# Optimization experiments

Measured on AMD Instinct MI355X. Metric: run time of the kernel, lower is better.

The kernel has to match this reference:

```python
import jax, jax.numpy as jnp
import numpy as np

N_NODES = 100000
N_EDGES = 1600000
IN_FEATS = 128
HIDDEN = 128
N_CLASSES = 40
EPS = 1e-5  # BatchNorm1d default eps


def setup_inputs():
    key = jax.random.key(0)
    ks = jax.random.split(key, 12)
    s_in = 1.0 / np.sqrt(IN_FEATS)
    s_h = 1.0 / np.sqrt(HIDDEN)
    return {
        "feat": jax.random.normal(ks[0], (N_NODES, IN_FEATS), jnp.float32),
        "src": jax.random.randint(ks[1], (N_EDGES,), 0, N_NODES, jnp.int32),
        "dst": jax.random.randint(ks[2], (N_EDGES,), 0, N_NODES, jnp.int32),
        # GraphConv weights, stored (out, in) as in the torch module
        "w0": jax.random.normal(ks[3], (HIDDEN, IN_FEATS), jnp.float32) * s_in,
        "w1": jax.random.normal(ks[4], (HIDDEN, HIDDEN), jnp.float32) * s_h,
        "w2": jax.random.normal(ks[5], (N_CLASSES, HIDDEN), jnp.float32) * s_h,
        "b2": jnp.zeros((N_CLASSES,), jnp.float32),  # bias only on last layer
        # skip-connection linears (use_linear=True, bias=False)
        "l0": jax.random.normal(ks[6], (HIDDEN, IN_FEATS), jnp.float32) * s_in,
        "l1": jax.random.normal(ks[7], (HIDDEN, HIDDEN), jnp.float32) * s_h,
        "l2": jax.random.normal(ks[8], (N_CLASSES, HIDDEN), jnp.float32) * s_h,
        # BatchNorm affine params for the two hidden layers
        "g0": jnp.ones((HIDDEN,), jnp.float32),
        "beta0": jnp.zeros((HIDDEN,), jnp.float32),
        "g1": jnp.ones((HIDDEN,), jnp.float32),
        "beta1": jnp.zeros((HIDDEN,), jnp.float32),
    }


def _spmm(h, src, dst):
    # copy_u + sum aggregation: out[d] = sum_{e: dst[e]==d} h[src[e]]
    return jax.ops.segment_sum(h[src], dst, num_segments=N_NODES)


def gcn_forward(feat, src, dst, w0, w1, w2, b2, l0, l1, l2, g0, beta0, g1, beta1):
    ones = jnp.ones((src.shape[0],), jnp.float32)
    out_deg = jnp.clip(jax.ops.segment_sum(ones, src, num_segments=N_NODES), 1.0)
    in_deg = jnp.clip(jax.ops.segment_sum(ones, dst, num_segments=N_NODES), 1.0)
    out_norm = out_deg ** -0.5  # norm='both', applied to src features
    in_norm = in_deg ** -0.5    # norm='both', applied to aggregated result

    def conv(h, W, bias, in_gt_out):
        hs = h * out_norm[:, None]
        if in_gt_out:  # in_feats > out_feats: project first, then aggregate
            rst = _spmm(hs @ W.T, src, dst)
        else:          # aggregate first, then project
            rst = _spmm(hs, src, dst) @ W.T
        rst = rst * in_norm[:, None]
        if bias is not None:
            rst = rst + bias
        return rst

    def bn(x, g, b):
        mu = x.mean(0)
        var = x.var(0)  # biased variance, matches BN training-mode normalization
        return (x - mu) * jax.lax.rsqrt(var + EPS) * g + b

    h = feat  # dropout in eval mode = identity
    h = jax.nn.relu(bn(conv(h, w0, None, IN_FEATS > HIDDEN) + h @ l0.T, g0, beta0))
    h = jax.nn.relu(bn(conv(h, w1, None, False) + h @ l1.T, g1, beta1))
    h = conv(h, w2, b2, HIDDEN > N_CLASSES) + h @ l2.T
    return h


def reference(feat, src, dst, w0, w1, w2, b2, l0, l1, l2, g0, beta0, g1, beta1):
    return gcn_forward(feat, src, dst, w0, w1, w2, b2, l0, l1, l2, g0, beta0, g1, beta1)
```

## Files before the change

### kernel.cpp

```cpp
#include <hip/hip_runtime.h>
#include <hip/hip_fp16.h>
#include <cstdint>
#include <cstddef>

#define N_NODES 100000
#define N_EDGES 1600000
#define EPS 1e-5f

typedef _Float16 half8 __attribute__((ext_vector_type(8)));
typedef float floatx4 __attribute__((ext_vector_type(4)));

#define HCH 128
#define HRG 4
#define HBINS 32768
#define HWORDS (HBINS / 2)
#define HCHUNK (N_EDGES / HCH)
#define HCHUNK4 (HCHUNK / 4)

__global__ void k_hist_part(const int* __restrict__ keys, unsigned int* __restrict__ Hpart) {
  __shared__ unsigned int bins[HWORDS];
  int c = blockIdx.x % HCH, r = blockIdx.x / HCH;
  int base = r * HBINS;
  for (int i = threadIdx.x; i < HWORDS; i += 256) bins[i] = 0;
  __syncthreads();
  const int4* k4 = (const int4*)(keys + c * HCHUNK);
  for (int i = threadIdx.x; i < HCHUNK4; i += 256) {
    int4 k = k4[i];
    int a;
    a = k.x - base; if ((unsigned)a < (unsigned)HBINS) atomicAdd(&bins[a >> 1], 1u << ((a & 1) * 16));
    a = k.y - base; if ((unsigned)a < (unsigned)HBINS) atomicAdd(&bins[a >> 1], 1u << ((a & 1) * 16));
    a = k.z - base; if ((unsigned)a < (unsigned)HBINS) atomicAdd(&bins[a >> 1], 1u << ((a & 1) * 16));
    a = k.w - base; if ((unsigned)a < (unsigned)HBINS) atomicAdd(&bins[a >> 1], 1u << ((a & 1) * 16));
  }
  __syncthreads();
  unsigned int* outp = Hpart + ((size_t)blockIdx.x << 14);
  for (int i = threadIdx.x; i < HWORDS; i += 256) outp[i] = bins[i];
}

__global__ void k_hist_sum(const unsigned short* __restrict__ Hp, int* __restrict__ deg) {
  int b = blockIdx.x * 256 + threadIdx.x;
  if (b >= N_NODES) return;
  int r = b >> 15, lo = b & (HBINS - 1);
  const unsigned short* p = Hp + ((size_t)(r * HCH) << 15) + lo;
  unsigned int t = 0;
#pragma unroll 8
  for (int c = 0; c < HCH; ++c) t += p[(size_t)c << 15];
  deg[b] = (int)t;
}

__global__ void k_hist_scan(unsigned short* __restrict__ Hp, int* __restrict__ degd) {
  int b = blockIdx.x * 256 + threadIdx.x;
  if (b >= N_NODES) return;
  int r = b >> 15, lo = b & (HBINS - 1);
  unsigned short* p = Hp + ((size_t)(r * HCH) << 15) + lo;
  unsigned int t = 0;
#pragma unroll 8
  for (int c = 0; c < HCH; ++c) {
    unsigned int v = p[(size_t)c << 15];
    p[(size_t)c << 15] = (unsigned short)t;
    t += v;
  }
  degd[b] = (int)t;
}

__global__ void k_build(const int* __restrict__ src, const int* __restrict__ dst,
                        const unsigned short* __restrict__ Hbase,
                        const int* __restrict__ row_start, int* __restrict__ col) {
  __shared__ unsigned int cur[HWORDS];
  int c = blockIdx.x % HCH, r = blockIdx.x / HCH;
  int base = r * HBINS;
  for (int i = threadIdx.x; i < HWORDS; i += 256) cur[i] = 0;
  __syncthreads();
  const unsigned short* hb = Hbase + ((size_t)blockIdx.x << 15);
  const int4* d4 = (const int4*)(dst + c * HCHUNK);
  const int4* s4 = (const int4*)(src + c * HCHUNK);
  for (int i = threadIdx.x; i < HCHUNK4; i += 256) {
    int4 d = d4[i];
    int4 s = s4[i];
    int a;
    a = d.x - base;
    if ((unsigned)a < (unsigned)HBINS) {
      unsigned old = atomicAdd(&cur[a >> 1], 1u << ((a & 1) * 16));
      unsigned lr = (old >> ((a & 1) * 16)) & 0xffffu;
      col[row_start[d.x] + hb[a] + lr] = s.x;
    }
    a = d.y - base;
    if ((unsigned)a < (unsigned)HBINS) {
      unsigned old = atomicAdd(&cur[a >> 1], 1u << ((a & 1) * 16));
      unsigned lr = (old >> ((a & 1) * 16)) & 0xffffu;
      col[row_start[d.y] + hb[a] + lr] = s.y;
    }
    a = d.z - base;
    if ((unsigned)a < (unsigned)HBINS) {
      unsigned old = atomicAdd(&cur[a >> 1], 1u << ((a & 1) * 16));
      unsigned lr = (old >> ((a & 1) * 16)) & 0xffffu;
      col[row_start[d.z] + hb[a] + lr] = s.z;
    }
    a = d.w - base;
    if ((unsigned)a < (unsigned)HBINS) {
      unsigned old = atomicAdd(&cur[a >> 1], 1u << ((a & 1) * 16));
      unsigned lr = (old >> ((a & 1) * 16)) & 0xffffu;
      col[row_start[d.w] + hb[a] + lr] = s.w;
    }
  }
}

__global__ void k_norms(const int* __restrict__ degs, const int* __restrict__ degd,
                        float* out_norm, float* in_norm) {
  int i = blockIdx.x * 256 + threadIdx.x;
  if (i < N_NODES) {
    out_norm[i] = rsqrtf((float)max(degs[i], 1));
    in_norm[i]  = rsqrtf((float)max(degd[i], 1));
  }
}

__global__ void k_scan1(const int* __restrict__ degd, int* bsum) {
  __shared__ int s[256];
  int t = threadIdx.x;
  int i = blockIdx.x * 256 + t;
  s[t] = (i < N_NODES) ? degd[i] : 0;
  __syncthreads();
  for (int off = 128; off > 0; off >>= 1) {
    if (t < off) s[t] += s[t + off];
    __syncthreads();
  }
  if (t == 0) bsum[blockIdx.x] = s[0];
}

__global__ void k_scan2(int* bsum, int nb) {
  __shared__ int s[512];
  int t = threadIdx.x;
  int v = (t < nb) ? bsum[t] : 0;
  s[t] = v;
  __syncthreads();
  for (int off = 1; off < 512; off <<= 1) {
    int x = (t >= off) ? s[t - off] : 0;
    __syncthreads();
    s[t] += x;
    __syncthreads();
  }
  if (t < nb) bsum[t] = s[t] - v;
}

__global__ void k_scan3(const int* __restrict__ degd, const int* __restrict__ bsum,
                        int* row_start) {
  __shared__ int s[256];
  int t = threadIdx.x;
  int i = blockIdx.x * 256 + t;
  int v = (i < N_NODES) ? degd[i] : 0;
  s[t] = v;
  __syncthreads();
  for (int off = 1; off < 256; off <<= 1) {
    int x = (t >= off) ? s[t - off] : 0;
    __syncthreads();
    s[t] += x;
    __syncthreads();
  }
  if (i < N_NODES) row_start[i] = bsum[blockIdx.x] + s[t] - v;
  if (i == 0) row_start[N_NODES] = N_EDGES;
}

__global__ void k_feat2h(const float* __restrict__ feat, const float* __restrict__ out_norm,
                         unsigned short* __restrict__ H, unsigned short* __restrict__ F) {
  int i = blockIdx.x * 256 + threadIdx.x;
  if (i >= N_NODES * 32) return;
  float on = out_norm[i >> 5];
  float4 v = ((const float4*)feat)[i];
  ushort4 s, u;
  s.x = __half_as_ushort(__float2half_rn(v.x * on));
  s.y = __half_as_ushort(__float2half_rn(v.y * on));
  s.z = __half_as_ushort(__float2half_rn(v.z * on));
  s.w = __half_as_ushort(__float2half_rn(v.w * on));
  u.x = __half_as_ushort(__float2half_rn(v.x));
  u.y = __half_as_ushort(__float2half_rn(v.y));
  u.z = __half_as_ushort(__float2half_rn(v.z));
  u.w = __half_as_ushort(__float2half_rn(v.w));
  ((ushort4*)H)[i] = s;
  ((ushort4*)F)[i] = u;
}

__global__ void k_agg128h(const __half* __restrict__ H, const int* __restrict__ col,
                          const int* __restrict__ row_start,
                          const float* __restrict__ in_norm,
                          unsigned short* __restrict__ out16) {
  int wave = threadIdx.x >> 6;
  int lane = threadIdx.x & 63;
  int node = blockIdx.x * 4 + wave;
  if (node >= N_NODES) return;
  int q = lane >> 4;
  int sub = lane & 15;
  int s0 = row_start[node], s1 = row_start[node + 1];
  const uint4* hp = (const uint4*)H;
  float a[8];
#pragma unroll
  for (int j = 0; j < 8; ++j) a[j] = 0.f;
  int e = s0 + q;
  for (; e + 4 < s1; e += 8) {
    int c0 = col[e];
    int c1 = col[e + 4];
    uint4 u0 = hp[(size_t)c0 * 16 + sub];
    uint4 u1 = hp[(size_t)c1 * 16 + sub];
    const __half2* h0 = (const __half2*)&u0;
    const __half2* h1 = (const __half2*)&u1;
#pragma unroll
    for (int j = 0; j < 4; ++j) {
      float2 f0 = __half22float2(h0[j]);
      float2 f1 = __half22float2(h1[j]);
      a[2 * j] += f0.x + f1.x;
      a[2 * j + 1] += f0.y + f1.y;
    }
  }
  if (e < s1) {
    uint4 u = hp[(size_t)col[e] * 16 + sub];
    const __half2* h0 = (const __half2*)&u;
#pragma unroll
    for (int j = 0; j < 4; ++j) {
      float2 f = __half22float2(h0[j]);
      a[2 * j] += f.x;
      a[2 * j + 1] += f.y;
    }
  }
#pragma unroll
  for (int j = 0; j < 8; ++j) {
    a[j] += __shfl_xor(a[j], 16);
    a[j] += __shfl_xor(a[j], 32);
  }
  if (q == 0) {
    float sc = in_norm[node];
    __half2 o[4];
#pragma unroll
    for (int j = 0; j < 4; ++j)
      o[j] = __float22half2_rn(make_float2(a[2 * j] * sc, a[2 * j + 1] * sc));
    ((uint4*)out16)[(size_t)node * 16 + sub] = *(const uint4*)o;
  }
}

__launch_bounds__(256)
__global__ void k_gemm_dual16(const unsigned short* __restrict__ Xa,
                              const unsigned short* __restrict__ Xh,
                              const float* __restrict__ Wa, const float* __restrict__ Wh,
                              unsigned short* __restrict__ Out16, float* __restrict__ stats) {
  __shared__ __align__(16) unsigned short sX[64][136];
  __shared__ __align__(16) unsigned short sW[128][136];
  int t = threadIdx.x;
  int row0 = blockIdx.x * 64;
  int w = t >> 6, lane = t & 63;
  int q = lane >> 4, m = lane & 15;
  floatx4 acc[8];
#pragma unroll
  for (int i = 0; i < 8; ++i) acc[i] = (floatx4){0.f, 0.f, 0.f, 0.f};

  for (int phase = 0; phase < 2; ++phase) {
    const unsigned short* Xg = phase ? Xh : Xa;
    const float* Wg = phase ? Wh : Wa;
    __syncthreads();
    {
      int r = t >> 2;
      int c0 = (t & 3) * 4;
      const uint4* xr = (const uint4*)(Xg + (size_t)min(row0 + r, N_NODES - 1) * 128);
#pragma unroll
      for (int it = 0; it < 4; ++it) {
        uint4 v = xr[c0 + it];
        *(uint4*)&sX[r][(c0 + it) * 8] = v;
      }
    }
    {
      int n = t >> 1, h = (t & 1) * 64;
      const float4* wr = (const float4*)(Wg + (size_t)n * 128 + h);
#pragma unroll
      for (int it = 0; it < 16; ++it) {
        float4 v = wr[it];
        ushort4 o;
        o.x = __half_as_ushort(__float2half_rn(v.x));
        o.y = __half_as_ushort(__float2half_rn(v.y));
        o.z = __half_as_ushort(__float2half_rn(v.z));
        o.w = __half_as_ushort(__float2half_rn(v.w));
        *(ushort4*)&sW[n][h + it * 4] = o;
      }
    }
    __syncthreads();
#pragma unroll
    for (int ks = 0; ks < 4; ++ks) {
      int kk = ks * 32 + q * 8;
      half8 a = *(const half8*)&sX[w * 16 + m][kk];
#pragma unroll
      for (int t8 = 0; t8 < 8; ++t8) {
        half8 b = *(const half8*)&sW[t8 * 16 + m][kk];
        acc[t8] = __builtin_amdgcn_mfma_f32_16x16x32_f16(a, b, acc[t8], 0, 0, 0);
      }
    }
  }
  float ps[8], pq[8];
#pragma unroll
  for (int t8 = 0; t8 < 8; ++t8) {
    int colj = t8 * 16 + m;
    float s = 0.f, sq = 0.f;
#pragma unroll
    for (int i = 0; i < 4; ++i) {
      int row = row0 + w * 16 + q * 4 + i;
      if (row < N_NODES) {
        float v = acc[t8][i];
        s += v; sq += v * v;
        Out16[(size_t)row * 128 + colj] = __half_as_ushort(__float2half_rn(v));
      }
    }
    s += __shfl_xor(s, 16);
    s += __shfl_xor(s, 32);
    sq += __shfl_xor(sq, 16);
    sq += __shfl_xor(sq, 32);
    ps[t8] = s; pq[t8] = sq;
  }
  __syncthreads();
  float* pSum = (float*)&sX[0][0];
  float* pSq = pSum + 512;
  if (q == 0) {
#pragma unroll
    for (int t8 = 0; t8 < 8; ++t8) {
      pSum[w * 128 + t8 * 16 + m] = ps[t8];
      pSq[w * 128 + t8 * 16 + m] = pq[t8];
    }
  }
  __syncthreads();
  if (t < 128) {
    float s = (pSum[t] + pSum[128 + t]) + (pSum[256 + t] + pSum[384 + t]);
    float sq = (pSq[t] + pSq[128 + t]) + (pSq[256 + t] + pSq[384 + t]);
    atomicAdd(&stats[t], s);
    atomicAdd(&stats[128 + t], sq);
  }
}

__global__ void k_bnrelu16(const unsigned short* __restrict__ x16,
                           const float* __restrict__ stats,
                           const float* __restrict__ g, const float* __restrict__ b,
                           const float* __restrict__ out_norm,
                           unsigned short* __restrict__ H, unsigned short* __restrict__ F) {
  int i = blockIdx.x * 256 + threadIdx.x;
  if (i >= N_NODES * 16) return;
  int c8 = (i & 15) * 8;
  uint4 raw = ((const uint4*)x16)[i];
  const __half2* hp2 = (const __half2*)&raw;
  float v[8];
#pragma unroll
  for (int j = 0; j < 4; ++j) {
    float2 f = __half22float2(hp2[j]);
    v[2 * j] = f.x;
    v[2 * j + 1] = f.y;
  }
  const float inv = 1.f / (float)N_NODES;
#pragma unroll
  for (int j = 0; j < 8; ++j) {
    int c = c8 + j;
    float mu = stats[c] * inv;
    float var = stats[128 + c] * inv - mu * mu;
    float rs = rsqrtf(var + EPS);
    float y = (v[j] - mu) * rs * g[c] + b[c];
    v[j] = y > 0.f ? y : 0.f;
  }
  if (H) {
    float on = out_norm[i >> 4];
    ushort4 o[2];
#pragma unroll
    for (int j = 0; j < 8; ++j) ((unsigned short*)o)[j] = __half_as_ushort(__float2half_rn(v[j] * on));
    ((uint4*)H)[i] = *(const uint4*)o;
  }
  if (F) {
    ushort4 o[2];
#pragma unroll
    for (int j = 0; j < 8; ++j) ((unsigned short*)o)[j] = __half_as_ushort(__float2half_rn(v[j]));
    ((uint4*)F)[i] = *(const uint4*)o;
  }
}

__launch_bounds__(256)
__global__ void k_gemm2_16(const unsigned short* __restrict__ X,
                           const float* __restrict__ w2, const float* __restrict__ l2,
                           const float* __restrict__ b2,
                           const float* __restrict__ out_norm,
                           __half* __restrict__ p, float* __restrict__ out) {
  __shared__ __align__(16) unsigned short sX[64][136];
  __shared__ __align__(16) unsigned short sW[80][136];
  int t = threadIdx.x;
  int row0 = blockIdx.x * 64;
  int w = t >> 6, lane = t & 63;
  int q = lane >> 4, m = lane & 15;
  {
    int r = t >> 2;
    int c0 = (t & 3) * 4;
    const uint4* xr = (const uint4*)(X + (size_t)min(row0 + r, N_NODES - 1) * 128);
#pragma unroll
    for (int it = 0; it < 4; ++it) {
      uint4 v = xr[c0 + it];
      *(uint4*)&sX[r][(c0 + it) * 8] = v;
    }
  }
  {
#pragma unroll
    for (int it = 0; it < 10; ++it) {
      int i = it * 256 + t;
      int j = i >> 5;
      int kq = i & 31;
      const float* srcp = (j < 40) ? (w2 + (size_t)j * 128) : (l2 + (size_t)(j - 40) * 128);
      float4 v = ((const float4*)srcp)[kq];
      ushort4 o;
      o.x = __half_as_ushort(__float2half_rn(v.x));
      o.y = __half_as_ushort(__float2half_rn(v.y));
      o.z = __half_as_ushort(__float2half_rn(v.z));
      o.w = __half_as_ushort(__float2half_rn(v.w));
      *(ushort4*)&sW[j][kq * 4] = o;
    }
  }
  __syncthreads();
  floatx4 acc[5];
#pragma unroll
  for (int i = 0; i < 5; ++i) acc[i] = (floatx4){0.f, 0.f, 0.f, 0.f};
#pragma unroll
  for (int ks = 0; ks < 4; ++ks) {
    int kk = ks * 32 + q * 8;
    half8 a = *(const half8*)&sX[w * 16 + m][kk];
#pragma unroll
    for (int t5 = 0; t5 < 5; ++t5) {
      half8 b = *(const half8*)&sW[t5 * 16 + m][kk];
      acc[t5] = __builtin_amdgcn_mfma_f32_16x16x32_f16(a, b, acc[t5], 0, 0, 0);
    }
  }
#pragma unroll
  for (int t5 = 0; t5 < 5; ++t5) {
    int col = t5 * 16 + m;
#pragma unroll
    for (int i = 0; i < 4; ++i) {
      int row = row0 + w * 16 + q * 4 + i;
      if (row >= N_NODES) continue;
      if (col < 40) {
        p[(size_t)row * 40 + col] = __float2half_rn(out_norm[row] * acc[t5][i]);
      } else {
        out[(size_t)row * 40 + (col - 40)] = acc[t5][i] + b2[col - 40];
      }
    }
  }
}

__global__ void k_agg40h(const __half* __restrict__ p, const int* __restrict__ col,
                         const int* __restrict__ row_start,
                         const float* __restrict__ in_norm,
                         float* __restrict__ out) {
  int wave = threadIdx.x >> 6, lane = threadIdx.x & 63;
  int node = blockIdx.x * 4 + wave;
  if (node >= N_NODES) return;
  int s0 = row_start[node], s1 = row_start[node + 1];
  float a0 = 0.f, a1 = 0.f, a2 = 0.f, a3 = 0.f;
  int e = s0;
  for (; e + 4 <= s1; e += 4) {
    int sA = col[e], sB = col[e + 1], sC = col[e + 2], sD = col[e + 3];
    float vA = __half2float(p[(size_t)sA * 40 + lane]);
    float vB = __half2float(p[(size_t)sB * 40 + lane]);
    float vC = __half2float(p[(size_t)sC * 40 + lane]);
    float vD = __half2float(p[(size_t)sD * 40 + lane]);
    a0 += vA; a1 += vB; a2 += vC; a3 += vD;
  }
  for (; e < s1; ++e) {
    a0 += __half2float(p[(size_t)col[e] * 40 + lane]);
  }
  if (lane < 40) out[(size_t)node * 40 + lane] += in_norm[node] * ((a0 + a1) + (a2 + a3));
}

extern "C" void kernel_launch(void* const* d_in, const int* in_sizes, int n_in,
                              void* d_out, int out_size, void* d_ws, size_t ws_size,
                              hipStream_t stream) {
  const float* feat = (const float*)d_in[0];
  const int* src = (const int*)d_in[1];
  const int* dst = (const int*)d_in[2];
  const float* w0 = (const float*)d_in[3];
  const float* w1 = (const float*)d_in[4];
  const float* w2 = (const float*)d_in[5];
  const float* b2 = (const float*)d_in[6];
  const float* l0 = (const float*)d_in[7];
  const float* l1 = (const float*)d_in[8];
  const float* l2 = (const float*)d_in[9];
  const float* g0 = (const float*)d_in[10];
  const float* beta0 = (const float*)d_in[11];
  const float* g1 = (const float*)d_in[12];
  const float* beta1 = (const float*)d_in[13];
  float* out = (float*)d_out;

  char* ws = (char*)d_ws;
  size_t off = 0;
  auto alloc = [&](size_t bytes) {
    void* ptr = ws + off;
    off = (off + bytes + 255) & ~(size_t)255;
    return ptr;
  };
  unsigned short* A16 = (unsigned short*)alloc(2 * (size_t)N_NODES * 128);
  float* B = (float*)alloc(sizeof(float) * (size_t)N_NODES * 128);
  unsigned short* H = (unsigned short*)alloc(2 * (size_t)N_NODES * 128);
  unsigned short* F = (unsigned short*)alloc(2 * (size_t)N_NODES * 128);
  int* degs = (int*)alloc(sizeof(int) * N_NODES);
  int* degd = (int*)alloc(sizeof(int) * N_NODES);
  int* row_start = (int*)alloc(sizeof(int) * (N_NODES + 1));
  int* colb = (int*)alloc(sizeof(int) * N_EDGES);
  float* out_norm = (float*)alloc(sizeof(float) * N_NODES);
  float* in_norm = (float*)alloc(sizeof(float) * N_NODES);
  int* bsum = (int*)alloc(sizeof(int) * 512);
  float* stats = (float*)alloc(sizeof(float) * 256);

  unsigned int* Hpart = (unsigned int*)B;
  unsigned short* B16 = (unsigned short*)B;

  int nb = (N_NODES + 255) / 256;
  int hb = HCH * HRG;

  k_hist_part<<<hb, 256, 0, stream>>>(src, Hpart);
  k_hist_sum<<<nb, 256, 0, stream>>>((const unsigned short*)Hpart, degs);
  k_hist_part<<<hb, 256, 0, stream>>>(dst, Hpart);
  k_hist_scan<<<nb, 256, 0, stream>>>((unsigned short*)Hpart, degd);
  k_norms<<<nb, 256, 0, stream>>>(degs, degd, out_norm, in_norm);
  k_scan1<<<nb, 256, 0, stream>>>(degd, bsum);
  k_scan2<<<1, 512, 0, stream>>>(bsum, nb);
  k_scan3<<<nb, 256, 0, stream>>>(degd, bsum, row_start);
  k_build<<<hb, 256, 0, stream>>>(src, dst, (const unsigned short*)Hpart, row_start, colb);

  int ab = (N_NODES + 3) / 4;
  int gb = (N_NODES + 63) / 64;
  int fb = (N_NODES * 32 + 255) / 256;
  int hb16 = (N_NODES * 16 + 255) / 256;

  k_feat2h<<<fb, 256, 0, stream>>>(feat, out_norm, H, F);
  k_agg128h<<<ab, 256, 0, stream>>>((const __half*)H, colb, row_start, in_norm, A16);
  hipMemsetAsync(stats, 0, sizeof(float) * 256, stream);
  k_gemm_dual16<<<gb, 256, 0, stream>>>(A16, F, w0, l0, B16, stats);
  k_bnrelu16<<<hb16, 256, 0, stream>>>(B16, stats, g0, beta0, out_norm, H, F);

  k_agg128h<<<ab, 256, 0, stream>>>((const __half*)H, colb, row_start, in_norm, A16);
  hipMemsetAsync(stats, 0, sizeof(float) * 256, stream);
  k_gemm_dual16<<<gb, 256, 0, stream>>>(A16, F, w1, l1, B16, stats);
  k_bnrelu16<<<hb16, 256, 0, stream>>>(B16, stats, g1, beta1, out_norm,
                                       (unsigned short*)nullptr, F);

  __half* p = (__half*)A16;
  k_gemm2_16<<<gb, 256, 0, stream>>>(F, w2, l2, b2, out_norm, p, out);
  k_agg40h<<<ab, 256, 0, stream>>>(p, colb, row_start, in_norm, out);
}
```

Measured before the change: 572.2 us.

## Pre-convert weights to fp16, two-stage BN stats, pad final aggregation rows to 64

Weights are converted to fp16 once in a small kernel, so the GEMM blocks no longer convert fp32 weights per block. BN statistics are written as per-block partials and reduced by a separate kernel instead of global atomics. Tile loads are reorganised so a wave reads contiguous rows. The final-layer intermediate is padded to 64 halves per row and aggregated with 16-byte vector loads, eight edges in parallel per wave. This adds two extra launches and extra bytes for the padding.

```diff
diff --git a/kernel.cpp b/kernel.cpp
--- a/kernel.cpp
+++ b/kernel.cpp
@@ -158,6 +158,29 @@
   }
   if (i < N_NODES) row_start[i] = bsum[blockIdx.x] + s[t] - v;
   if (i == 0) row_start[N_NODES] = N_EDGES;
+}
+
+__global__ void k_w2h(const float* __restrict__ w0, const float* __restrict__ l0,
+                      const float* __restrict__ w1, const float* __restrict__ l1,
+                      const float* __restrict__ w2, const float* __restrict__ l2,
+                      unsigned short* __restrict__ W) {
+  int i = blockIdx.x * 256 + threadIdx.x;
+  if (i >= 18944) return;
+  int h = i * 4;
+  const float* src; int off;
+  if (h < 16384)      { src = w0; off = h; }
+  else if (h < 32768) { src = l0; off = h - 16384; }
+  else if (h < 49152) { src = w1; off = h - 32768; }
+  else if (h < 65536) { src = l1; off = h - 49152; }
+  else if (h < 70656) { src = w2; off = h - 65536; }
+  else                { src = l2; off = h - 70656; }
+  float4 v = *(const float4*)(src + off);
+  ushort4 o;
+  o.x = __half_as_ushort(__float2half_rn(v.x));
+  o.y = __half_as_ushort(__float2half_rn(v.y));
+  o.z = __half_as_ushort(__float2half_rn(v.z));
+  o.w = __half_as_ushort(__float2half_rn(v.w));
+  ((ushort4*)W)[i] = o;
 }
 
 __global__ void k_feat2h(const float* __restrict__ feat, const float* __restrict__ out_norm,
@@ -238,8 +261,8 @@
 __launch_bounds__(256)
 __global__ void k_gemm_dual16(const unsigned short* __restrict__ Xa,
                               const unsigned short* __restrict__ Xh,
-                              const float* __restrict__ Wa, const float* __restrict__ Wh,
-                              unsigned short* __restrict__ Out16, float* __restrict__ stats) {
+                              const unsigned short* __restrict__ W16,
+                              unsigned short* __restrict__ Out16, float* __restrict__ pstats) {
   __shared__ __align__(16) unsigned short sX[64][136];
   __shared__ __align__(16) unsigned short sW[128][136];
   int t = threadIdx.x;
@@ -252,30 +275,23 @@
 
   for (int phase = 0; phase < 2; ++phase) {
     const unsigned short* Xg = phase ? Xh : Xa;
-    const float* Wg = phase ? Wh : Wa;
     __syncthreads();
     {
-      int r = t >> 2;
-      int c0 = (t & 3) * 4;
-      const uint4* xr = (const uint4*)(Xg + (size_t)min(row0 + r, N_NODES - 1) * 128);
 #pragma unroll
       for (int it = 0; it < 4; ++it) {
-        uint4 v = xr[c0 + it];
-        *(uint4*)&sX[r][(c0 + it) * 8] = v;
+        int idx = it * 256 + t;
+        int r = idx >> 4, g = idx & 15;
+        const uint4* xr = (const uint4*)(Xg + (size_t)min(row0 + r, N_NODES - 1) * 128);
+        *(uint4*)&sX[r][g * 8] = xr[g];
       }
     }
     {
-      int n = t >> 1, h = (t & 1) * 64;
-      const float4* wr = (const float4*)(Wg + (size_t)n * 128 + h);
-#pragma unroll
-      for (int it = 0; it < 16; ++it) {
-        float4 v = wr[it];
-        ushort4 o;
-        o.x = __half_as_ushort(__float2half_rn(v.x));
-        o.y = __half_as_ushort(__float2half_rn(v.y));
-        o.z = __half_as_ushort(__float2half_rn(v.z));
-        o.w = __half_as_ushort(__float2half_rn(v.w));
-        *(ushort4*)&sW[n][h + it * 4] = o;
+      const uint4* wsrc = (const uint4*)(W16 + ((size_t)phase << 14));
+#pragma unroll
+      for (int it = 0; it < 8; ++it) {
+        int idx = it * 256 + t;
+        int n = idx >> 4, g = idx & 15;
+        *(uint4*)&sW[n][g * 8] = wsrc[idx];
       }
     }
     __syncthreads();
@@ -324,9 +340,18 @@
   if (t < 128) {
     float s = (pSum[t] + pSum[128 + t]) + (pSum[256 + t] + pSum[384 + t]);
     float sq = (pSq[t] + pSq[128 + t]) + (pSq[256 + t] + pSq[384 + t]);
-    atomicAdd(&stats[t], s);
-    atomicAdd(&stats[128 + t], sq);
-  }
+    pstats[(size_t)blockIdx.x * 256 + t] = s;
+    pstats[(size_t)blockIdx.x * 256 + 128 + t] = sq;
+  }
+}
+
+__global__ void k_stats_red(const float* __restrict__ pstats, float* __restrict__ stats,
+                            int nblk) {
+  int t = threadIdx.x;
+  float s = 0.f;
+  for (int b = blockIdx.x; b < nblk; b += gridDim.x)
+    s += pstats[(size_t)b * 256 + t];
+  atomicAdd(&stats[t], s);
 }
 
 __global__ void k_bnrelu16(const unsigned short* __restrict__ x16,
@@ -373,7 +398,7 @@
 
 __launch_bounds__(256)
 __global__ void k_gemm2_16(const unsigned short* __restrict__ X,
-                           const float* __restrict__ w2, const float* __restrict__ l2,
+                           const unsigned short* __restrict__ W80,
                            const float* __restrict__ b2,
                            const float* __restrict__ out_norm,
                            __half* __restrict__ p, float* __restrict__ out) {
@@ -384,29 +409,21 @@
   int w = t >> 6, lane = t & 63;
   int q = lane >> 4, m = lane & 15;
   {
-    int r = t >> 2;
-    int c0 = (t & 3) * 4;
-    const uint4* xr = (const uint4*)(X + (size_t)min(row0 + r, N_NODES - 1) * 128);
 #pragma unroll
     for (int it = 0; it < 4; ++it) {
-      uint4 v = xr[c0 + it];
-      *(uint4*)&sX[r][(c0 + it) * 8] = v;
+      int idx = it * 256 + t;
+      int r = idx >> 4, g = idx & 15;
+      const uint4* xr = (const uint4*)(X + (size_t)min(row0 + r, N_NODES - 1) * 128);
+      *(uint4*)&sX[r][g * 8] = xr[g];
     }
   }
   {
-#pragma unroll
-    for (int it = 0; it < 10; ++it) {
-      int i = it * 256 + t;
-      int j = i >> 5;
-      int kq = i & 31;
-      const float* srcp = (j < 40) ? (w2 + (size_t)j * 128) : (l2 + (size_t)(j - 40) * 128);
-      float4 v = ((const float4*)srcp)[kq];
-      ushort4 o;
-      o.x = __half_as_ushort(__float2half_rn(v.x));
-      o.y = __half_as_ushort(__float2half_rn(v.y));
-      o.z = __half_as_ushort(__float2half_rn(v.z));
-      o.w = __half_as_ushort(__float2half_rn(v.w));
-      *(ushort4*)&sW[j][kq * 4] = o;
+    const uint4* wsrc = (const uint4*)W80;
+#pragma unroll
+    for (int it = 0; it < 5; ++it) {
+      int idx = it * 256 + t;
+      int n = idx >> 4, g = idx & 15;
+      *(uint4*)&sW[n][g * 8] = wsrc[idx];
     }
   }
   __syncthreads();
@@ -431,36 +448,73 @@
       int row = row0 + w * 16 + q * 4 + i;
       if (row >= N_NODES) continue;
       if (col < 40) {
-        p[(size_t)row * 40 + col] = __float2half_rn(out_norm[row] * acc[t5][i]);
+        p[(size_t)row * 64 + col] = __float2half_rn(out_norm[row] * acc[t5][i]);
       } else {
         out[(size_t)row * 40 + (col - 40)] = acc[t5][i] + b2[col - 40];
       }
     }
   }
-}
-
-__global__ void k_agg40h(const __half* __restrict__ p, const int* __restrict__ col,
+  for (int idx = t; idx < 64 * 24; idx += 256) {
+    int r = idx / 24, c = 40 + idx % 24;
+    int row = row0 + r;
+    if (row < N_NODES) p[(size_t)row * 64 + c] = __float2half_rn(0.f);
+  }
+}
+
+__global__ void k_agg64h(const __half* __restrict__ p, const int* __restrict__ col,
                          const int* __restrict__ row_start,
                          const float* __restrict__ in_norm,
                          float* __restrict__ out) {
   int wave = threadIdx.x >> 6, lane = threadIdx.x & 63;
   int node = blockIdx.x * 4 + wave;
   if (node >= N_NODES) return;
+  int oct = lane >> 3;
+  int sub = lane & 7;
   int s0 = row_start[node], s1 = row_start[node + 1];
-  float a0 = 0.f, a1 = 0.f, a2 = 0.f, a3 = 0.f;
-  int e = s0;
-  for (; e + 4 <= s1; e += 4) {
-    int sA = col[e], sB = col[e + 1], sC = col[e + 2], sD = col[e + 3];
-    float vA = __half2float(p[(size_t)sA * 40 + lane]);
-    float vB = __half2float(p[(size_t)sB * 40 + lane]);
-    float vC = __half2float(p[(size_t)sC * 40 + lane]);
-    float vD = __half2float(p[(size_t)sD * 40 + lane]);
-    a0 += vA; a1 += vB; a2 += vC; a3 += vD;
-  }
-  for (; e < s1; ++e) {
-    a0 += __half2float(p[(size_t)col[e] * 40 + lane]);
-  }
-  if (lane < 40) out[(size_t)node * 40 + lane] += in_norm[node] * ((a0 + a1) + (a2 + a3));
+  const uint4* pp = (const uint4*)p;
+  float a[8];
+#pragma unroll
+  for (int j = 0; j < 8; ++j) a[j] = 0.f;
+  int e = s0 + oct;
+  for (; e + 8 < s1; e += 16) {
+    int c0 = col[e];
+    int c1 = col[e + 8];
+    uint4 u0 = pp[(size_t)c0 * 8 + sub];
+    uint4 u1 = pp[(size_t)c1 * 8 + sub];
+    const __half2* h0 = (const __half2*)&u0;
+    const __half2* h1 = (const __half2*)&u1;
+#pragma unroll
+    for (int j = 0; j < 4; ++j) {
+      float2 f0 = __half22float2(h0[j]);
+      float2 f1 = __half22float2(h1[j]);
+      a[2 * j] += f0.x + f1.x;
+      a[2 * j + 1] += f0.y + f1.y;
+    }
+  }
+  if (e < s1) {
+    uint4 u = pp[(size_t)col[e] * 8 + sub];
+    const __half2* h0 = (const __half2*)&u;
+#pragma unroll
+    for (int j = 0; j < 4; ++j) {
+      float2 f = __half22float2(h0[j]);
+      a[2 * j] += f.x;
+      a[2 * j + 1] += f.y;
+    }
+  }
+#pragma unroll
+  for (int j = 0; j < 8; ++j) {
+    a[j] += __shfl_xor(a[j], 8);
+    a[j] += __shfl_xor(a[j], 16);
+    a[j] += __shfl_xor(a[j], 32);
+  }
+  if (oct == 0 && sub < 5) {
+    float sc = in_norm[node];
+    float4* op = (float4*)(out + (size_t)node * 40 + (size_t)sub * 8);
+    float4 v0 = op[0], v1 = op[1];
+    v0.x += sc * a[0]; v0.y += sc * a[1]; v0.z += sc * a[2]; v0.w += sc * a[3];
+    v1.x += sc * a[4]; v1.y += sc * a[5]; v1.z += sc * a[6]; v1.w += sc * a[7];
+    op[0] = v0; op[1] = v1;
+  }
 }
 
 extern "C" void kernel_launch(void* const* d_in, const int* in_sizes, int n_in,
@@ -501,12 +555,17 @@
   float* in_norm = (float*)alloc(sizeof(float) * N_NODES);
   int* bsum = (int*)alloc(sizeof(int) * 512);
   float* stats = (float*)alloc(sizeof(float) * 256);
+  unsigned short* W16 = (unsigned short*)alloc(2 * (size_t)75776);
+  int gb = (N_NODES + 63) / 64;
+  float* pstats = (float*)alloc(sizeof(float) * (size_t)gb * 256);
 
   unsigned int* Hpart = (unsigned int*)B;
   unsigned short* B16 = (unsigned short*)B;
 
   int nb = (N_NODES + 255) / 256;
   int hb = HCH * HRG;
+
+  k_w2h<<<74, 256, 0, stream>>>(w0, l0, w1, l1, w2, l2, W16);
 
   k_hist_part<<<hb, 256, 0, stream>>>(src, Hpart);
   k_hist_sum<<<nb, 256, 0, stream>>>((const unsigned short*)Hpart, degs);
@@ -519,23 +578,24 @@
   k_build<<<hb, 256, 0, stream>>>(src, dst, (const unsigned short*)Hpart, row_start, colb);
 
   int ab = (N_NODES + 3) / 4;
-  int gb = (N_NODES + 63) / 64;
   int fb = (N_NODES * 32 + 255) / 256;
   int hb16 = (N_NODES * 16 + 255) / 256;
 
   k_feat2h<<<fb, 256, 0, stream>>>(feat, out_norm, H, F);
   k_agg128h<<<ab, 256, 0, stream>>>((const __half*)H, colb, row_start, in_norm, A16);
+  k_gemm_dual16<<<gb, 256, 0, stream>>>(A16, F, W16, B16, pstats);
   hipMemsetAsync(stats, 0, sizeof(float) * 256, stream);
-  k_gemm_dual16<<<gb, 256, 0, stream>>>(A16, F, w0, l0, B16, stats);
+  k_stats_red<<<32, 256, 0, stream>>>(pstats, stats, gb);
   k_bnrelu16<<<hb16, 256, 0, stream>>>(B16, stats, g0, beta0, out_norm, H, F);
 
   k_agg128h<<<ab, 256, 0, stream>>>((const __half*)H, colb, row_start, in_norm, A16);
+  k_gemm_dual16<<<gb, 256, 0, stream>>>(A16, F, W16 + 32768, B16, pstats);
   hipMemsetAsync(stats, 0, sizeof(float) * 256, stream);
-  k_gemm_dual16<<<gb, 256, 0, stream>>>(A16, F, w1, l1, B16, stats);
+  k_stats_red<<<32, 256, 0, stream>>>(pstats, stats, gb);
   k_bnrelu16<<<hb16, 256, 0, stream>>>(B16, stats, g1, beta1, out_norm,
                                        (unsigned short*)nullptr, F);
 
   __half* p = (__half*)A16;
-  k_gemm2_16<<<gb, 256, 0, stream>>>(F, w2, l2, b2, out_norm, p, out);
-  k_agg40h<<<ab, 256, 0, stream>>>(p, colb, row_start, in_norm, out);
-}
+  k_gemm2_16<<<gb, 256, 0, stream>>>(F, W16 + 65536, b2, out_norm, p, out);
+  k_agg64h<<<ab, 256, 0, stream>>>(p, colb, row_start, in_norm, out);
+}
```

Measured after the change: 509.8 us. 10.9% less time.
